# Kernel tuning notes

Hardware: AMD Instinct MI355X
Metric: run time of the kernel (lower is better)

Reference implementation:

```python
import jax, jax.numpy as jnp
import numpy as np

DT = 0.2
T = 30
SIZE_TAB = [10, 1024, 1024, 784]
BATCH = 256

def rho(x):
    # hard-sigmoid nonlinearity used throughout the EP/SNN codebase
    return jnp.clip(x, 0.0, 1.0)

def setup_inputs() -> dict:
    key = jax.random.key(0)
    ks = jax.random.split(key, 8)
    data = jax.random.uniform(ks[0], (BATCH, SIZE_TAB[3]), dtype=jnp.float32)
    s0 = jnp.zeros((BATCH, SIZE_TAB[0]), jnp.float32)
    s1 = jnp.zeros((BATCH, SIZE_TAB[1]), jnp.float32)
    s2 = jnp.zeros((BATCH, SIZE_TAB[2]), jnp.float32)
    def lin(k, out_d, in_d):
        bound = 1.0 / np.sqrt(in_d)
        return jax.random.uniform(k, (out_d, in_d), jnp.float32, -bound, bound)
    # w0: size_tab[1]->size_tab[0] (bias), w1 = w0.T (no bias)
    W0 = lin(ks[1], SIZE_TAB[0], SIZE_TAB[1]); b0 = jnp.zeros((SIZE_TAB[0],), jnp.float32)
    W1 = W0.T  # transpose init, faithful to __init__
    # w2: size_tab[2]->size_tab[1] (bias), w3 = w2.T (no bias)
    W2 = lin(ks[2], SIZE_TAB[1], SIZE_TAB[2]); b2 = jnp.zeros((SIZE_TAB[1],), jnp.float32)
    W3 = W2.T
    # w4 (= w[-1]): size_tab[3]->size_tab[2], default bias
    W4 = lin(ks[3], SIZE_TAB[2], SIZE_TAB[3]); b4 = jnp.zeros((SIZE_TAB[2],), jnp.float32)
    return {"data": data, "s0": s0, "s1": s1, "s2": s2,
            "W0": W0, "b0": b0, "W1": W1, "W2": W2, "b2": b2,
            "W3": W3, "W4": W4, "b4": b4}

def reference(data, s0, s1, s2, W0, b0, W1, W2, b2, W3, W4, b4):
    # Free phase (beta=0): T Euler steps of the leaky-integrator SNN.
    base = jax.random.key(42)
    def step(carry, t):
        s0, s1, s2 = carry
        k = jax.random.fold_in(base, t)
        k0, k1, k2 = jax.random.split(k, 3)
        # bernoulli spikes: rand < rho(s)
        sp0 = (jax.random.uniform(k0, s0.shape) < rho(s0)).astype(s0.dtype)
        sp1 = (jax.random.uniform(k1, s1.shape) < rho(s1)).astype(s1.dtype)
        sp2 = (jax.random.uniform(k2, s2.shape) < rho(s2)).astype(s2.dtype)
        # dsdt computed from pre-update states (as in torch)
        ds0 = -s0 + sp1 @ W0.T + b0
        ds1 = -s1 + sp2 @ W2.T + b2 + sp0 @ W1.T
        ds2 = -s2 + data @ W4.T + b4 + rho(s1) @ W3.T  # last layer uses s (not spikes) from data layer
        n0 = jnp.clip(s0 + DT * ds0, 0.0, 1.0)
        n1 = jnp.clip(s1 + DT * ds1, 0.0, 1.0)
        n2 = jnp.clip(s2 + DT * ds2, 0.0, 1.0)
        return (n0, n1, n2), None
    (s0, s1, s2), _ = jax.lax.scan(step, (s0, s1, s2), jnp.arange(T))
    return s0, s1, s2, data  # s[-1] (data layer) is never updated
```

## Files before the change

### kernel.cpp

```cpp
#include <hip/hip_runtime.h>
#include <stdint.h>

#define DTv 0.2f

typedef __attribute__((ext_vector_type(8))) short short8;
typedef __attribute__((ext_vector_type(4))) float f32x4;
#define MFMA16(A,B,C) __builtin_amdgcn_mfma_f32_16x16x32_bf16(A,B,C,0,0,0)
#define GLOAD16(gp, lp) __builtin_amdgcn_global_load_lds( \
    (const __attribute__((address_space(1))) void*)(gp), \
    (__attribute__((address_space(3))) void*)(lp), 16, 0, 0)

__device__ __forceinline__ void st_u16_sc(ushort* p, uint v){
  asm volatile("global_store_short %0, %1, off sc0 sc1" :: "v"(p), "v"(v) : "memory");
}
__device__ __forceinline__ void st_u32_sc(uint* p, uint v){
  asm volatile("global_store_dword %0, %1, off sc0 sc1" :: "v"(p), "v"(v) : "memory");
}
__device__ __forceinline__ void st_f32_sc(float* p, float v){
  asm volatile("global_store_dword %0, %1, off sc0 sc1" :: "v"(p), "v"(v) : "memory");
}

__device__ __forceinline__ uint32_t rotl32(uint32_t v, uint32_t r){ return (v<<r)|(v>>(32u-r)); }

__device__ __forceinline__ void tf2x32(uint32_t k0, uint32_t k1, uint32_t& x0, uint32_t& x1){
  const uint32_t k2 = k0 ^ k1 ^ 0x1BD11BDAu;
  x0 += k0; x1 += k1;
#define RND(r) { x0 += x1; x1 = rotl32(x1,(r)); x1 ^= x0; }
  RND(13u) RND(15u) RND(26u) RND(6u)
  x0 += k1; x1 += k2 + 1u;
  RND(17u) RND(29u) RND(16u) RND(24u)
  x0 += k2; x1 += k0 + 2u;
  RND(13u) RND(15u) RND(26u) RND(6u)
  x0 += k0; x1 += k1 + 3u;
  RND(17u) RND(29u) RND(16u) RND(24u)
  x0 += k1; x1 += k2 + 4u;
  RND(13u) RND(15u) RND(26u) RND(6u)
  x0 += k2; x1 += k0 + 5u;
#undef RND
}

__device__ __forceinline__ float u01(uint32_t bits){
  return __uint_as_float((bits >> 9) | 0x3f800000u) - 1.0f;
}

__device__ __forceinline__ void step_keys(int t, uint32_t* K){
  uint32_t c0 = 0u, c1 = (uint32_t)t;
  tf2x32(0u, 42u, c0, c1);
#pragma unroll
  for (int i = 0; i < 3; ++i){
    uint32_t a = 0u, b = (uint32_t)i;
    tf2x32(c0, c1, a, b);
    K[2*i] = a; K[2*i+1] = b;
  }
}

__device__ __forceinline__ ushort f2bf(float f){
  uint32_t u = __float_as_uint(f);
  u += 0x7fffu + ((u >> 16) & 1u);
  return (ushort)(u >> 16);
}
__device__ __forceinline__ float bf2f(ushort h){ return __uint_as_float(((uint32_t)h) << 16); }

__global__ __launch_bounds__(256) void d2p_kernel(
    const float* __restrict__ data, const float* __restrict__ W4, float* __restrict__ Pd2)
{
  __shared__ float As[16][64];
  __shared__ float Bs[16][64];
  const int tb = blockIdx.x / 7;
  const int ch = blockIdx.x % 7;
  const int kb = ch * 112;
  const int R0 = (tb >> 4) << 6;
  const int C0 = (tb & 15) << 6;
  const int tid = threadIdx.x;
  const int ty = tid >> 4, tx = tid & 15;
  const int mA = tid >> 2, kqA = (tid & 3) << 2;
  float acc[4][4] = {{0.f}};
  for (int kk = 0; kk < 112; kk += 16){
    const float4 a = *(const float4*)&data[(R0+mA)*784 + kb + kk + kqA];
    As[kqA+0][mA]=a.x; As[kqA+1][mA]=a.y; As[kqA+2][mA]=a.z; As[kqA+3][mA]=a.w;
    const float4 b = *(const float4*)&W4[(C0+mA)*784 + kb + kk + kqA];
    Bs[kqA+0][mA]=b.x; Bs[kqA+1][mA]=b.y; Bs[kqA+2][mA]=b.z; Bs[kqA+3][mA]=b.w;
    __syncthreads();
#pragma unroll
    for (int k=0;k<16;k++){
      const float4 av = *(const float4*)&As[k][ty<<2];
      const float4 bv = *(const float4*)&Bs[k][tx<<2];
      acc[0][0]=fmaf(av.x,bv.x,acc[0][0]); acc[0][1]=fmaf(av.x,bv.y,acc[0][1]);
      acc[0][2]=fmaf(av.x,bv.z,acc[0][2]); acc[0][3]=fmaf(av.x,bv.w,acc[0][3]);
      acc[1][0]=fmaf(av.y,bv.x,acc[1][0]); acc[1][1]=fmaf(av.y,bv.y,acc[1][1]);
      acc[1][2]=fmaf(av.y,bv.z,acc[1][2]); acc[1][3]=fmaf(av.y,bv.w,acc[1][3]);
      acc[2][0]=fmaf(av.z,bv.x,acc[2][0]); acc[2][1]=fmaf(av.z,bv.y,acc[2][1]);
      acc[2][2]=fmaf(av.z,bv.z,acc[2][2]); acc[2][3]=fmaf(av.z,bv.w,acc[2][3]);
      acc[3][0]=fmaf(av.w,bv.x,acc[3][0]); acc[3][1]=fmaf(av.w,bv.y,acc[3][1]);
      acc[3][2]=fmaf(av.w,bv.z,acc[3][2]); acc[3][3]=fmaf(av.w,bv.w,acc[3][3]);
    }
    __syncthreads();
  }
  float* P = Pd2 + ch*262144;
#pragma unroll
  for (int i=0;i<4;i++){
    const int r = R0 + (ty<<2) + i;
    float4 o; float* op=(float*)&o;
#pragma unroll
    for (int j=0;j<4;j++) op[j] = acc[i][j];
    *(float4*)&P[r*1024 + C0 + (tx<<2)] = o;
  }
}

__global__ __launch_bounds__(256) void d2r_kernel(
    const float* __restrict__ Pd2, const float* __restrict__ b4, float* __restrict__ D2)
{
  const int e = (blockIdx.x*256 + threadIdx.x) << 2;
  float4 acc = *(const float4*)&Pd2[e];
#pragma unroll
  for (int p = 1; p < 7; ++p){
    const float4 q = *(const float4*)&Pd2[p*262144 + e];
    acc.x += q.x; acc.y += q.y; acc.z += q.z; acc.w += q.w;
  }
  const float4 bb = *(const float4*)&b4[e & 1023];
  acc.x += bb.x; acc.y += bb.y; acc.z += bb.z; acc.w += bb.w;
  *(float4*)&D2[e] = acc;
}

__device__ __forceinline__ void arrive(unsigned* xbar, unsigned* cnt, int grp, unsigned a){
  const unsigned old = __hip_atomic_fetch_add(&xbar[grp << 5], 1u,
                        __ATOMIC_RELAXED, __HIP_MEMORY_SCOPE_AGENT);
  if (old == a*32u + 31u)
    __hip_atomic_fetch_add(cnt, 1u, __ATOMIC_RELAXED, __HIP_MEMORY_SCOPE_AGENT);
}
__device__ __forceinline__ void spinwait(unsigned* cnt, unsigned target){
  unsigned it = 0;
  while (__hip_atomic_load(cnt, __ATOMIC_RELAXED, __HIP_MEMORY_SCOPE_AGENT) < target){
    __builtin_amdgcn_s_sleep(2);
    if (++it > (1u<<26)) break;
  }
  __builtin_amdgcn_fence(__ATOMIC_ACQUIRE, "agent");
}

__global__ __launch_bounds__(512) void persist_kernel(
    const float* __restrict__ data, const float* __restrict__ s0i,
    const float* __restrict__ s1i, const float* __restrict__ s2i,
    const float* __restrict__ W1g, const float* __restrict__ W2,
    const float* __restrict__ W3, const float* __restrict__ b0g,
    const float* __restrict__ b2g, const float* __restrict__ D2,
    float* __restrict__ sp0A, float* __restrict__ sp0B,
    unsigned* __restrict__ sp1bA, unsigned* __restrict__ sp1bB,
    unsigned* __restrict__ sp2bA, unsigned* __restrict__ sp2bB,
    ushort* __restrict__ ahA, ushort* __restrict__ ahB,
    ushort* __restrict__ alA, ushort* __restrict__ alB,
    float* __restrict__ out, unsigned* __restrict__ bar)
{
  extern __shared__ char lds[];
  short* Bh   = (short*)lds;
  short* Bl   = (short*)(lds + 32768);
  short* Abuf = (short*)(lds + 65536);
  float* Sst  = (float*)(lds + 131072);
  float* AUX  = (float*)(lds + 139264);
  float* MISC = (float*)(lds + 147456);
  uint32_t* K  = (uint32_t*)MISC;
  float* b0s   = MISC + 8;
  float* s0st  = MISC + 18;
  float* s0red = MISC + 38;
  float* b2s   = MISC + 120;
  float* W1epi = MISC + 136;

  unsigned* xbar = bar;
  unsigned* cA   = bar + 256;
  unsigned* cB   = bar + 320;

  const int bid = blockIdx.x, tid = threadIdx.x;
  const int grp = bid & 7;
  const int g2 = (bid >> 2) & 1, sub = (bid >> 1) & 1;
  const int coltile = ((bid & 1) << 5) + (bid >> 3);
  const int cb = coltile << 4;
  const int w = tid >> 6, lane = tid & 63, lr = lane & 15, sl = lane >> 4;
  const int r0s = ((coltile << 1) + sub) << 1;

  {
    const float* Wsrc = g2 ? W3 : W2;
    const int row = tid >> 5, seg = tid & 31;
    const float* src = &Wsrc[(cb + row)*1024 + seg*32];
#pragma unroll
    for (int g = 0; g < 4; ++g){
      short8 h8, l8;
#pragma unroll
      for (int j = 0; j < 8; ++j){
        const float f = src[g*8 + j];
        const ushort hh = f2bf(f);
        h8[j] = (short)hh;
        l8[j] = (short)f2bf(f - bf2f(hh));
      }
      const int kg = seg*4 + g;
      *(short8*)&Bh[(kg<<7) + (row<<3)] = h8;
      *(short8*)&Bl[(kg<<7) + (row<<3)] = l8;
    }
  }
  for (int i = tid; i < 160; i += 512) W1epi[i] = W1g[(cb + i/10)*10 + (i%10)];
  float w1c[20];
#pragma unroll
  for (int j = 0; j < 10; ++j){
    w1c[j]      = W1g[tid*10 + j];
    w1c[10 + j] = W1g[(tid + 512)*10 + j];
  }
  {
    const float* Ssrc = g2 ? s2i : s1i;
    for (int idx = tid; idx < 2048; idx += 512){
      const int r = idx >> 4, c = idx & 15;
      Sst[idx] = Ssrc[(((sub<<7)+r)<<10) + cb + c];
    }
    if (g2){
      for (int idx = tid; idx < 2048; idx += 512){
        const int r = idx >> 4, c = idx & 15;
        AUX[idx] = D2[(((sub<<7)+r)<<10) + cb + c];
      }
    }
  }
  if (tid < 10) b0s[tid] = b0g[tid];
  if (g2 && tid < 20) s0st[tid] = s0i[(r0s + tid/10)*10 + (tid%10)];
  if (tid < 16) b2s[tid] = b2g[cb + tid];
  for (int idx = tid; idx < 784; idx += 512)
    out[526848 + bid*784 + idx] = data[bid*784 + idx];
  if (tid == 0) step_keys(0, K);
  __syncthreads();

  {
    const uint32_t kk0 = g2 ? K[4] : K[2];
    const uint32_t kk1 = g2 ? K[5] : K[3];
    ushort* sp1u = (ushort*)sp1bA;
    ushort* sp2u = (ushort*)sp2bA;
#pragma unroll
    for (int i2 = 0; i2 < 4; ++i2){
      const int rloc = (w<<4) + (sl<<2) + i2;
      const int R = (sub<<7) + rloc;
      const int e = (R << 10) + cb + lr;
      const float v = fminf(fmaxf(Sst[(rloc<<4) + lr], 0.f), 1.f);
      uint32_t x0 = 0u, x1 = (uint32_t)e;
      tf2x32(kk0, kk1, x0, x1);
      const bool sp = (u01(x0 ^ x1) < v);
      const unsigned long long bt = __ballot(sp ? 1 : 0);
      if (!g2){
        const int hh = (int)f2bf(v);
        const int ll = (int)f2bf(v - bf2f((ushort)hh));
        const int hp = __shfl_down(hh, 1);
        const int lp = __shfl_down(ll, 1);
        if (!(lr & 1)){
          st_u32_sc((uint*)&ahA[e], (uint)(ushort)hh | ((uint)(ushort)hp << 16));
          st_u32_sc((uint*)&alA[e], (uint)(ushort)ll | ((uint)(ushort)lp << 16));
        }
        if (lr == 0) st_u16_sc(&sp1u[R*64 + (cb>>4)], (uint)((bt >> (sl<<4)) & 0xFFFFu));
      } else {
        if (lr == 0) st_u16_sc(&sp2u[R*64 + (cb>>4)], (uint)((bt >> (sl<<4)) & 0xFFFFu));
      }
    }
    if (g2 && tid < 20){
      const float v = fminf(fmaxf(s0st[tid], 0.f), 1.f);
      const int e = (r0s + tid/10)*10 + (tid%10);
      uint32_t x0 = 0u, x1 = (uint32_t)e;
      tf2x32(K[0], K[1], x0, x1);
      st_f32_sc(&sp0A[e], (u01(x0 ^ x1) < v) ? 1.0f : 0.0f);
    }
  }
  asm volatile("s_waitcnt vmcnt(0)" ::: "memory");
  __syncthreads();
  if (tid == 0) arrive(xbar, g2 ? cB : cA, grp, 0u);

  const int r0g = (sub << 7) + (w << 4);
  const int gbase = ((r0g + (lane >> 2)) << 10) + ((((lane & 3) ^ ((lane >> 2) & 3))) << 3);
  const int fragoff = (lr << 5) + ((sl ^ (lr & 3)) << 3);
  const int shl = sl << 3;
  short* AW = Abuf + (w << 12);

#pragma unroll 1
  for (int t = 0; t < 30; ++t){
    const int cur = t & 1;
    const float*    sp0c  = cur ? sp0B  : sp0A;   float*    sp0n  = cur ? sp0A  : sp0B;
    const unsigned* sp1bc = cur ? sp1bB : sp1bA;  unsigned* sp1bn = cur ? sp1bA : sp1bB;
    const unsigned* sp2bc = cur ? sp2bB : sp2bA;  unsigned* sp2bn = cur ? sp2bA : sp2bB;
    const ushort*   ahc   = cur ? ahB   : ahA;    ushort*   ahn   = cur ? ahA   : ahB;
    const ushort*   alc   = cur ? alB   : alA;    ushort*   aln   = cur ? alA   : alB;

    if (tid == 0){
      step_keys(t+1, K);
      spinwait(g2 ? cA : cB, 4u*(t+1));
    }
    __syncthreads();

    if (!g2){
      for (int idx = tid; idx < 1280; idx += 512) AUX[idx] = sp0c[sub*1280 + idx];
      __syncthreads();
    } else {
#pragma unroll 1
      for (int rr = 0; rr < 2; ++rr){
        const int r = r0s + rr;
        const unsigned* mrow = sp1bc + r*32;
        const unsigned d0 = mrow[tid >> 5];
        const unsigned d1 = mrow[16 + (tid >> 5)];
        const float sv0 = (float)((d0 >> (tid & 31)) & 1u);
        const float sv1 = (float)((d1 >> (tid & 31)) & 1u);
        float a0_[10];
#pragma unroll
        for (int c2 = 0; c2 < 10; ++c2){
          float a = fmaf(sv0, w1c[c2], 0.f);
          a0_[c2] = fmaf(sv1, w1c[10 + c2], a);
        }
#pragma unroll
        for (int c2 = 0; c2 < 10; ++c2){
          float v = a0_[c2];
          v += __shfl_xor(v, 1);  v += __shfl_xor(v, 2);  v += __shfl_xor(v, 4);
          v += __shfl_xor(v, 8);  v += __shfl_xor(v, 16); v += __shfl_xor(v, 32);
          a0_[c2] = v;
        }
        if (lane == 0){
#pragma unroll
          for (int c2 = 0; c2 < 10; ++c2) s0red[w*10 + c2] = a0_[c2];
        }
        __syncthreads();
        if (tid < 10){
          float sum = 0.f;
#pragma unroll
          for (int ww = 0; ww < 8; ++ww) sum += s0red[ww*10 + tid];
          const float s = s0st[rr*10 + tid];
          float nv = s + DTv*(-s + sum + b0s[tid]);
          nv = fminf(fmaxf(nv, 0.f), 1.f);
          s0st[rr*10 + tid] = nv;
          const int e = r*10 + tid;
          uint32_t x0 = 0u, x1 = (uint32_t)e;
          tf2x32(K[0], K[1], x0, x1);
          st_f32_sc(&sp0n[e], (u01(x0 ^ x1) < nv) ? 1.0f : 0.0f);
        }
        __syncthreads();
      }
    }

    f32x4 acc0 = {0.f,0.f,0.f,0.f}, acc1 = {0.f,0.f,0.f,0.f}, acc2 = {0.f,0.f,0.f,0.f};
    if (!g2){
      const unsigned* mrow = sp2bc + (r0g + lr)*32;
      const uint4 m0 = *(const uint4*)(mrow +  0);
      const uint4 m1 = *(const uint4*)(mrow +  4);
      const uint4 m2 = *(const uint4*)(mrow +  8);
      const uint4 m3 = *(const uint4*)(mrow + 12);
      const uint4 m4 = *(const uint4*)(mrow + 16);
      const uint4 m5 = *(const uint4*)(mrow + 20);
      const uint4 m6 = *(const uint4*)(mrow + 24);
      const uint4 m7 = *(const uint4*)(mrow + 28);
#define U0(ks, DW) { \
      const unsigned b_ = ((DW) >> shl) & 0xFFu; \
      short8 a8; \
      a8[0]=(short)(((b_    )&1)?0x3F80:0); a8[1]=(short)(((b_>>1)&1)?0x3F80:0); \
      a8[2]=(short)(((b_>>2)&1)?0x3F80:0); a8[3]=(short)(((b_>>3)&1)?0x3F80:0); \
      a8[4]=(short)(((b_>>4)&1)?0x3F80:0); a8[5]=(short)(((b_>>5)&1)?0x3F80:0); \
      a8[6]=(short)(((b_>>6)&1)?0x3F80:0); a8[7]=(short)(((b_>>7)&1)?0x3F80:0); \
      const int ib = ((((ks)<<2)+sl)<<7) + (lr<<3); \
      const short8 bh8 = *(const short8*)(Bh + ib); \
      const short8 bl8 = *(const short8*)(Bl + ib); \
      acc0 = MFMA16(a8, bh8, acc0); \
      acc1 = MFMA16(a8, bl8, acc1); }
      U0(0,m0.x)  U0(1,m0.y)  U0(2,m0.z)  U0(3,m0.w)
      U0(4,m1.x)  U0(5,m1.y)  U0(6,m1.z)  U0(7,m1.w)
      U0(8,m2.x)  U0(9,m2.y)  U0(10,m2.z) U0(11,m2.w)
      U0(12,m3.x) U0(13,m3.y) U0(14,m3.z) U0(15,m3.w)
      U0(16,m4.x) U0(17,m4.y) U0(18,m4.z) U0(19,m4.w)
      U0(20,m5.x) U0(21,m5.y) U0(22,m5.z) U0(23,m5.w)
      U0(24,m6.x) U0(25,m6.y) U0(26,m6.z) U0(27,m6.w)
      U0(28,m7.x) U0(29,m7.y) U0(30,m7.z) U0(31,m7.w)
#undef U0
    } else {
      const short* Ah0 = (const short*)ahc + gbase;
      const short* Al0 = (const short*)alc + gbase;
#define G1_ISSUE(c) { GLOAD16(Ah0 + ((c)<<5), AW + (((c)&3)<<10)); \
                      GLOAD16(Al0 + ((c)<<5), AW + (((c)&3)<<10) + 512); }
#define G1_ITER(c, vm) { \
      asm volatile("s_waitcnt vmcnt(" #vm ")" ::: "memory"); \
      __builtin_amdgcn_sched_barrier(0); \
      const short8 h8  = *(const short8*)(AW + (((c)&3)<<10) + fragoff); \
      const short8 l8  = *(const short8*)(AW + (((c)&3)<<10) + 512 + fragoff); \
      const int ib = ((((c)<<2)+sl)<<7) + (lr<<3); \
      const short8 bh8 = *(const short8*)(Bh + ib); \
      const short8 bl8 = *(const short8*)(Bl + ib); \
      acc0 = MFMA16(h8, bh8, acc0); \
      acc1 = MFMA16(h8, bl8, acc1); \
      acc2 = MFMA16(l8, bh8, acc2); \
      __builtin_amdgcn_sched_barrier(0); \
      if ((c) < 28) G1_ISSUE((c)+4) }
      G1_ISSUE(0) G1_ISSUE(1) G1_ISSUE(2) G1_ISSUE(3)
      G1_ITER(0,6)  G1_ITER(1,6)  G1_ITER(2,6)  G1_ITER(3,6)
      G1_ITER(4,6)  G1_ITER(5,6)  G1_ITER(6,6)  G1_ITER(7,6)
      G1_ITER(8,6)  G1_ITER(9,6)  G1_ITER(10,6) G1_ITER(11,6)
      G1_ITER(12,6) G1_ITER(13,6) G1_ITER(14,6) G1_ITER(15,6)
      G1_ITER(16,6) G1_ITER(17,6) G1_ITER(18,6) G1_ITER(19,6)
      G1_ITER(20,6) G1_ITER(21,6) G1_ITER(22,6) G1_ITER(23,6)
      G1_ITER(24,6) G1_ITER(25,6) G1_ITER(26,6) G1_ITER(27,6)
      G1_ITER(28,6) G1_ITER(29,4) G1_ITER(30,2) G1_ITER(31,0)
#undef G1_ITER
#undef G1_ISSUE
    }

    {
      const bool emit = (t < 29);
      if (!g2){
        const uint32_t kk0 = K[2], kk1 = K[3];
        ushort* sp1u = (ushort*)sp1bn;
#pragma unroll
        for (int i2 = 0; i2 < 4; ++i2){
          const int rloc = (w<<4) + (sl<<2) + i2;
          float v = acc0[i2] + acc1[i2];
          float sm = 0.f;
#pragma unroll
          for (int k2 = 0; k2 < 10; ++k2)
            sm = fmaf(AUX[rloc*10 + k2], W1epi[lr*10 + k2], sm);
          v += b2s[lr] + sm;
          const float s = Sst[(rloc<<4) + lr];
          float nv = s + DTv*(-s + v);
          nv = fminf(fmaxf(nv, 0.f), 1.f);
          Sst[(rloc<<4) + lr] = nv;
          if (emit){
            const int R = (sub<<7) + rloc;
            const int e = (R << 10) + cb + lr;
            uint32_t x0 = 0u, x1 = (uint32_t)e;
            tf2x32(kk0, kk1, x0, x1);
            const bool sp = (u01(x0 ^ x1) < nv);
            const int hh = (int)f2bf(nv);
            const int ll = (int)f2bf(nv - bf2f((ushort)hh));
            const int hp = __shfl_down(hh, 1);
            const int lp = __shfl_down(ll, 1);
            if (!(lr & 1)){
              st_u32_sc((uint*)&ahn[e], (uint)(ushort)hh | ((uint)(ushort)hp << 16));
              st_u32_sc((uint*)&aln[e], (uint)(ushort)ll | ((uint)(ushort)lp << 16));
            }
            const unsigned long long bt = __ballot(sp ? 1 : 0);
            if (lr == 0) st_u16_sc(&sp1u[R*64 + (cb>>4)], (uint)((bt >> (sl<<4)) & 0xFFFFu));
          }
        }
      } else {
        const uint32_t kk0 = K[4], kk1 = K[5];
        ushort* sp2u = (ushort*)sp2bn;
#pragma unroll
        for (int i2 = 0; i2 < 4; ++i2){
          const int rloc = (w<<4) + (sl<<2) + i2;
          float v = acc0[i2] + acc1[i2] + acc2[i2];
          v += AUX[(rloc<<4) + lr];
          const float s = Sst[(rloc<<4) + lr];
          float nv = s + DTv*(-s + v);
          nv = fminf(fmaxf(nv, 0.f), 1.f);
          Sst[(rloc<<4) + lr] = nv;
          if (emit){
            const int R = (sub<<7) + rloc;
            const int e = (R << 10) + cb + lr;
            uint32_t x0 = 0u, x1 = (uint32_t)e;
            tf2x32(kk0, kk1, x0, x1);
            const bool sp = (u01(x0 ^ x1) < nv);
            const unsigned long long bt = __ballot(sp ? 1 : 0);
            if (lr == 0) st_u16_sc(&sp2u[R*64 + (cb>>4)], (uint)((bt >> (sl<<4)) & 0xFFFFu));
          }
        }
      }
    }

    asm volatile("s_waitcnt vmcnt(0)" ::: "memory");
    __syncthreads();
    if (tid == 0 && t < 29) arrive(xbar, g2 ? cB : cA, grp, (unsigned)(t+1));
  }

  __syncthreads();
  for (int idx = tid; idx < 2048; idx += 512){
    const int r = (sub<<7) + (idx >> 4);
    const int c = cb + (idx & 15);
    out[(g2 ? 264704 : 2560) + (r << 10) + c] = Sst[idx];
  }
  if (g2 && tid < 20) out[(r0s + tid/10)*10 + (tid%10)] = s0st[tid];
}

extern "C" void kernel_launch(void* const* d_in, const int* in_sizes, int n_in,
                              void* d_out, int out_size, void* d_ws, size_t ws_size,
                              hipStream_t stream)
{
  const float* data = (const float*)d_in[0];
  const float* s0i  = (const float*)d_in[1];
  const float* s1i  = (const float*)d_in[2];
  const float* s2i  = (const float*)d_in[3];
  const float* b0   = (const float*)d_in[5];
  const float* W1   = (const float*)d_in[6];
  const float* W2   = (const float*)d_in[7];
  const float* b2   = (const float*)d_in[8];
  const float* W3   = (const float*)d_in[9];
  const float* W4   = (const float*)d_in[10];
  const float* b4   = (const float*)d_in[11];
  float* out = (float*)d_out;
  float* ws  = (float*)d_ws;

  float* sp0A = ws + 0;
  float* sp0B = ws + 2560;
  float* D2   = ws + 5120;
  float* Pd2  = ws + 267264;
  ushort* ahA = (ushort*)(ws + 2102272);
  ushort* ahB = (ushort*)(ws + 2233344);
  ushort* alA = (ushort*)(ws + 2364416);
  ushort* alB = (ushort*)(ws + 2495488);
  unsigned* sp1bA = (unsigned*)(ws + 2626560);
  unsigned* sp1bB = (unsigned*)(ws + 2634752);
  unsigned* sp2bA = (unsigned*)(ws + 2642944);
  unsigned* sp2bB = (unsigned*)(ws + 2651136);
  unsigned* bar   = (unsigned*)(ws + 2659328);

  hipMemsetAsync(bar, 0, 2048, stream);
  d2p_kernel<<<448,256,0,stream>>>(data, W4, Pd2);
  d2r_kernel<<<256,256,0,stream>>>(Pd2, b4, D2);
  persist_kernel<<<256,512,149504,stream>>>(
      data, s0i, s1i, s2i, W1, W2, W3, b0, b2, D2,
      sp0A, sp0B, sp1bA, sp1bB, sp2bA, sp2bB,
      ahA, ahB, alA, alB, out, bar);
}
```

Baseline: 455.4 us.

## Load A fragments directly to registers and move layer-0 work to s1 blocks

New measurement: 561.6 us. 1.23x slower.

```diff
diff --git a/kernel.cpp b/kernel.cpp
--- a/kernel.cpp
+++ b/kernel.cpp
@@ -6,9 +6,6 @@
 typedef __attribute__((ext_vector_type(8))) short short8;
 typedef __attribute__((ext_vector_type(4))) float f32x4;
 #define MFMA16(A,B,C) __builtin_amdgcn_mfma_f32_16x16x32_bf16(A,B,C,0,0,0)
-#define GLOAD16(gp, lp) __builtin_amdgcn_global_load_lds( \
-    (const __attribute__((address_space(1))) void*)(gp), \
-    (__attribute__((address_space(3))) void*)(lp), 16, 0, 0)
 
 __device__ __forceinline__ void st_u16_sc(ushort* p, uint v){
   asm volatile("global_store_short %0, %1, off sc0 sc1" :: "v"(p), "v"(v) : "memory");
@@ -19,6 +16,10 @@
 __device__ __forceinline__ void st_f32_sc(float* p, float v){
   asm volatile("global_store_dword %0, %1, off sc0 sc1" :: "v"(p), "v"(v) : "memory");
 }
+
+#define LDA16(dst, base, OFF) \
+  asm volatile("global_load_dwordx4 %0, %1, off offset:" #OFF \
+               : "=v"(dst) : "v"(base) : "memory");
 
 __device__ __forceinline__ uint32_t rotl32(uint32_t v, uint32_t r){ return (v<<r)|(v>>(32u-r)); }
 
@@ -153,10 +154,8 @@
   extern __shared__ char lds[];
   short* Bh   = (short*)lds;
   short* Bl   = (short*)(lds + 32768);
-  short* Abuf = (short*)(lds + 65536);
-  float* Sst  = (float*)(lds + 131072);
-  float* AUX  = (float*)(lds + 139264);
-  float* MISC = (float*)(lds + 147456);
+  float* AUX  = (float*)(lds + 65536);
+  float* MISC = (float*)(lds + 73728);
   uint32_t* K  = (uint32_t*)MISC;
   float* b0s   = MISC + 8;
   float* s0st  = MISC + 18;
@@ -175,6 +174,9 @@
   const int cb = coltile << 4;
   const int w = tid >> 6, lane = tid & 63, lr = lane & 15, sl = lane >> 4;
   const int r0s = ((coltile << 1) + sub) << 1;
+  const int r0g = (sub << 7) + (w << 4);
+  const int aoff = ((r0g + lr) << 10) + (sl << 3);
+  const int shl = sl << 3;
 
   {
     const float* Wsrc = g2 ? W3 : W2;
@@ -197,26 +199,26 @@
   }
   for (int i = tid; i < 160; i += 512) W1epi[i] = W1g[(cb + i/10)*10 + (i%10)];
   float w1c[20];
-#pragma unroll
-  for (int j = 0; j < 10; ++j){
-    w1c[j]      = W1g[tid*10 + j];
-    w1c[10 + j] = W1g[(tid + 512)*10 + j];
-  }
+  if (!g2){
+#pragma unroll
+    for (int j = 0; j < 10; ++j){
+      w1c[j]      = W1g[tid*10 + j];
+      w1c[10 + j] = W1g[(tid + 512)*10 + j];
+    }
+  }
+  float sst[4], d2reg[4];
   {
     const float* Ssrc = g2 ? s2i : s1i;
-    for (int idx = tid; idx < 2048; idx += 512){
-      const int r = idx >> 4, c = idx & 15;
-      Sst[idx] = Ssrc[(((sub<<7)+r)<<10) + cb + c];
-    }
-    if (g2){
-      for (int idx = tid; idx < 2048; idx += 512){
-        const int r = idx >> 4, c = idx & 15;
-        AUX[idx] = D2[(((sub<<7)+r)<<10) + cb + c];
-      }
+#pragma unroll
+    for (int i2 = 0; i2 < 4; ++i2){
+      const int rloc = (w<<4) + (sl<<2) + i2;
+      const int e = (((sub<<7) + rloc) << 10) + cb + lr;
+      sst[i2] = Ssrc[e];
+      d2reg[i2] = g2 ? D2[e] : 0.f;
     }
   }
   if (tid < 10) b0s[tid] = b0g[tid];
-  if (g2 && tid < 20) s0st[tid] = s0i[(r0s + tid/10)*10 + (tid%10)];
+  if (!g2 && tid < 20) s0st[tid] = s0i[(r0s + tid/10)*10 + (tid%10)];
   if (tid < 16) b2s[tid] = b2g[cb + tid];
   for (int idx = tid; idx < 784; idx += 512)
     out[526848 + bid*784 + idx] = data[bid*784 + idx];
@@ -233,7 +235,7 @@
       const int rloc = (w<<4) + (sl<<2) + i2;
       const int R = (sub<<7) + rloc;
       const int e = (R << 10) + cb + lr;
-      const float v = fminf(fmaxf(Sst[(rloc<<4) + lr], 0.f), 1.f);
+      const float v = fminf(fmaxf(sst[i2], 0.f), 1.f);
       uint32_t x0 = 0u, x1 = (uint32_t)e;
       tf2x32(kk0, kk1, x0, x1);
       const bool sp = (u01(x0 ^ x1) < v);
@@ -252,7 +254,7 @@
         if (lr == 0) st_u16_sc(&sp2u[R*64 + (cb>>4)], (uint)((bt >> (sl<<4)) & 0xFFFFu));
       }
     }
-    if (g2 && tid < 20){
+    if (!g2 && tid < 20){
       const float v = fminf(fmaxf(s0st[tid], 0.f), 1.f);
       const int e = (r0s + tid/10)*10 + (tid%10);
       uint32_t x0 = 0u, x1 = (uint32_t)e;
@@ -263,12 +265,6 @@
   asm volatile("s_waitcnt vmcnt(0)" ::: "memory");
   __syncthreads();
   if (tid == 0) arrive(xbar, g2 ? cB : cA, grp, 0u);
-
-  const int r0g = (sub << 7) + (w << 4);
-  const int gbase = ((r0g + (lane >> 2)) << 10) + ((((lane & 3) ^ ((lane >> 2) & 3))) << 3);
-  const int fragoff = (lr << 5) + ((sl ^ (lr & 3)) << 3);
-  const int shl = sl << 3;
-  short* AW = Abuf + (w << 12);
 
 #pragma unroll 1
   for (int t = 0; t < 30; ++t){
@@ -285,16 +281,16 @@
     }
     __syncthreads();
 
+    f32x4 acc0 = {0.f,0.f,0.f,0.f}, acc1 = {0.f,0.f,0.f,0.f}, acc2 = {0.f,0.f,0.f,0.f};
     if (!g2){
       for (int idx = tid; idx < 1280; idx += 512) AUX[idx] = sp0c[sub*1280 + idx];
       __syncthreads();
-    } else {
 #pragma unroll 1
       for (int rr = 0; rr < 2; ++rr){
         const int r = r0s + rr;
-        const unsigned* mrow = sp1bc + r*32;
-        const unsigned d0 = mrow[tid >> 5];
-        const unsigned d1 = mrow[16 + (tid >> 5)];
+        const unsigned* mrow0 = sp1bc + r*32;
+        const unsigned d0 = mrow0[tid >> 5];
+        const unsigned d1 = mrow0[16 + (tid >> 5)];
         const float sv0 = (float)((d0 >> (tid & 31)) & 1u);
         const float sv1 = (float)((d1 >> (tid & 31)) & 1u);
         float a0_[10];
@@ -330,10 +326,6 @@
         }
         __syncthreads();
       }
-    }
-
-    f32x4 acc0 = {0.f,0.f,0.f,0.f}, acc1 = {0.f,0.f,0.f,0.f}, acc2 = {0.f,0.f,0.f,0.f};
-    if (!g2){
       const unsigned* mrow = sp2bc + (r0g + lr)*32;
       const uint4 m0 = *(const uint4*)(mrow +  0);
       const uint4 m1 = *(const uint4*)(mrow +  4);
@@ -365,34 +357,54 @@
       U0(28,m7.x) U0(29,m7.y) U0(30,m7.z) U0(31,m7.w)
 #undef U0
     } else {
-      const short* Ah0 = (const short*)ahc + gbase;
-      const short* Al0 = (const short*)alc + gbase;
-#define G1_ISSUE(c) { GLOAD16(Ah0 + ((c)<<5), AW + (((c)&3)<<10)); \
-                      GLOAD16(Al0 + ((c)<<5), AW + (((c)&3)<<10) + 512); }
-#define G1_ITER(c, vm) { \
+      const short* pAh = (const short*)ahc + aoff;
+      const short* pAl = (const short*)alc + aoff;
+      short8 hbuf[4], lbuf[4];
+#define G1_ISS(c, OFF) { LDA16(hbuf[(c)&3], pAh, OFF) LDA16(lbuf[(c)&3], pAl, OFF) }
+#define G1_IT(c, vm) { \
       asm volatile("s_waitcnt vmcnt(" #vm ")" ::: "memory"); \
       __builtin_amdgcn_sched_barrier(0); \
-      const short8 h8  = *(const short8*)(AW + (((c)&3)<<10) + fragoff); \
-      const short8 l8  = *(const short8*)(AW + (((c)&3)<<10) + 512 + fragoff); \
+      const short8 h8 = hbuf[(c)&3]; \
+      const short8 l8 = lbuf[(c)&3]; \
       const int ib = ((((c)<<2)+sl)<<7) + (lr<<3); \
       const short8 bh8 = *(const short8*)(Bh + ib); \
       const short8 bl8 = *(const short8*)(Bl + ib); \
       acc0 = MFMA16(h8, bh8, acc0); \
       acc1 = MFMA16(h8, bl8, acc1); \
       acc2 = MFMA16(l8, bh8, acc2); \
-      __builtin_amdgcn_sched_barrier(0); \
-      if ((c) < 28) G1_ISSUE((c)+4) }
-      G1_ISSUE(0) G1_ISSUE(1) G1_ISSUE(2) G1_ISSUE(3)
-      G1_ITER(0,6)  G1_ITER(1,6)  G1_ITER(2,6)  G1_ITER(3,6)
-      G1_ITER(4,6)  G1_ITER(5,6)  G1_ITER(6,6)  G1_ITER(7,6)
-      G1_ITER(8,6)  G1_ITER(9,6)  G1_ITER(10,6) G1_ITER(11,6)
-      G1_ITER(12,6) G1_ITER(13,6) G1_ITER(14,6) G1_ITER(15,6)
-      G1_ITER(16,6) G1_ITER(17,6) G1_ITER(18,6) G1_ITER(19,6)
-      G1_ITER(20,6) G1_ITER(21,6) G1_ITER(22,6) G1_ITER(23,6)
-      G1_ITER(24,6) G1_ITER(25,6) G1_ITER(26,6) G1_ITER(27,6)
-      G1_ITER(28,6) G1_ITER(29,4) G1_ITER(30,2) G1_ITER(31,0)
-#undef G1_ITER
-#undef G1_ISSUE
+      __builtin_amdgcn_sched_barrier(0); }
+      G1_ISS(0,0) G1_ISS(1,64) G1_ISS(2,128) G1_ISS(3,192)
+      G1_IT(0,6)  G1_ISS(4,256)
+      G1_IT(1,6)  G1_ISS(5,320)
+      G1_IT(2,6)  G1_ISS(6,384)
+      G1_IT(3,6)  G1_ISS(7,448)
+      G1_IT(4,6)  G1_ISS(8,512)
+      G1_IT(5,6)  G1_ISS(9,576)
+      G1_IT(6,6)  G1_ISS(10,640)
+      G1_IT(7,6)  G1_ISS(11,704)
+      G1_IT(8,6)  G1_ISS(12,768)
+      G1_IT(9,6)  G1_ISS(13,832)
+      G1_IT(10,6) G1_ISS(14,896)
+      G1_IT(11,6) G1_ISS(15,960)
+      G1_IT(12,6) G1_ISS(16,1024)
+      G1_IT(13,6) G1_ISS(17,1088)
+      G1_IT(14,6) G1_ISS(18,1152)
+      G1_IT(15,6) G1_ISS(19,1216)
+      G1_IT(16,6) G1_ISS(20,1280)
+      G1_IT(17,6) G1_ISS(21,1344)
+      G1_IT(18,6) G1_ISS(22,1408)
+      G1_IT(19,6) G1_ISS(23,1472)
+      G1_IT(20,6) G1_ISS(24,1536)
+      G1_IT(21,6) G1_ISS(25,1600)
+      G1_IT(22,6) G1_ISS(26,1664)
+      G1_IT(23,6) G1_ISS(27,1728)
+      G1_IT(24,6) G1_ISS(28,1792)
+      G1_IT(25,6) G1_ISS(29,1856)
+      G1_IT(26,6) G1_ISS(30,1920)
+      G1_IT(27,6) G1_ISS(31,1984)
+      G1_IT(28,6) G1_IT(29,4) G1_IT(30,2) G1_IT(31,0)
+#undef G1_IT
+#undef G1_ISS
     }
 
     {
@@ -409,10 +421,10 @@
           for (int k2 = 0; k2 < 10; ++k2)
             sm = fmaf(AUX[rloc*10 + k2], W1epi[lr*10 + k2], sm);
           v += b2s[lr] + sm;
-          const float s = Sst[(rloc<<4) + lr];
+          const float s = sst[i2];
           float nv = s + DTv*(-s + v);
           nv = fminf(fmaxf(nv, 0.f), 1.f);
-          Sst[(rloc<<4) + lr] = nv;
+          sst[i2] = nv;
           if (emit){
             const int R = (sub<<7) + rloc;
             const int e = (R << 10) + cb + lr;
@@ -438,11 +450,11 @@
         for (int i2 = 0; i2 < 4; ++i2){
           const int rloc = (w<<4) + (sl<<2) + i2;
           float v = acc0[i2] + acc1[i2] + acc2[i2];
-          v += AUX[(rloc<<4) + lr];
-          const float s = Sst[(rloc<<4) + lr];
+          v += d2reg[i2];
+          const float s = sst[i2];
           float nv = s + DTv*(-s + v);
           nv = fminf(fmaxf(nv, 0.f), 1.f);
-          Sst[(rloc<<4) + lr] = nv;
+          sst[i2] = nv;
           if (emit){
             const int R = (sub<<7) + rloc;
             const int e = (R << 10) + cb + lr;
@@ -461,13 +473,13 @@
     if (tid == 0 && t < 29) arrive(xbar, g2 ? cB : cA, grp, (unsigned)(t+1));
   }
 
-  __syncthreads();
-  for (int idx = tid; idx < 2048; idx += 512){
-    const int r = (sub<<7) + (idx >> 4);
-    const int c = cb + (idx & 15);
-    out[(g2 ? 264704 : 2560) + (r << 10) + c] = Sst[idx];
-  }
-  if (g2 && tid < 20) out[(r0s + tid/10)*10 + (tid%10)] = s0st[tid];
+#pragma unroll
+  for (int i2 = 0; i2 < 4; ++i2){
+    const int rloc = (w<<4) + (sl<<2) + i2;
+    const int e = (((sub<<7) + rloc) << 10) + cb + lr;
+    out[(g2 ? 264704 : 2560) + e] = sst[i2];
+  }
+  if (!g2 && tid < 20) out[(r0s + tid/10)*10 + (tid%10)] = s0st[tid];
 }
 
 extern "C" void kernel_launch(void* const* d_in, const int* in_sizes, int n_in,
@@ -505,7 +517,7 @@
   hipMemsetAsync(bar, 0, 2048, stream);
   d2p_kernel<<<448,256,0,stream>>>(data, W4, Pd2);
   d2r_kernel<<<256,256,0,stream>>>(Pd2, b4, D2);
-  persist_kernel<<<256,512,149504,stream>>>(
+  persist_kernel<<<256,512,75264,stream>>>(
       data, s0i, s1i, s2i, W1, W2, W3, b0, b2, D2,
       sp0A, sp0B, sp1bA, sp1bB, sp2bA, sp2bB,
       ahA, ahB, alA, alB, out, bar);
```
